# Performance work log

Measured on AMD Instinct MI355X. Metric: run time of the kernel, lower is better.

Reference implementation:

```python
import jax, jax.numpy as jnp
import numpy as np

HIDDEN = 768
NUM_HEADS = 12
HEAD_DIM = HIDDEN // NUM_HEADS


def setup_inputs() -> dict:
    key = jax.random.key(0)
    ks = jax.random.split(key, 10)
    B, S = 4, 2048
    scale = 1.0 / np.sqrt(HIDDEN)
    inp = {
        "hidden_states": jax.random.normal(ks[0], (B, S, HIDDEN), dtype=jnp.float32),
        "attention_mask": jnp.ones((B, S), dtype=jnp.float32),
        "Wq": jax.random.normal(ks[1], (HIDDEN, HIDDEN), dtype=jnp.float32) * scale,
        "bq": jnp.zeros((HIDDEN,), dtype=jnp.float32),
        "Wk": jax.random.normal(ks[2], (HIDDEN, HIDDEN), dtype=jnp.float32) * scale,
        "bk": jnp.zeros((HIDDEN,), dtype=jnp.float32),
        "Wv": jax.random.normal(ks[3], (HIDDEN, HIDDEN), dtype=jnp.float32) * scale,
        "bv": jnp.zeros((HIDDEN,), dtype=jnp.float32),
        "Wo": jax.random.normal(ks[4], (HIDDEN, HIDDEN), dtype=jnp.float32) * scale,
        "bo": jnp.zeros((HIDDEN,), dtype=jnp.float32),
    }
    return inp


def _split_heads(x):
    # [B,S,H] -> [B,nh,S,dh]
    B, S, _ = x.shape
    return x.reshape(B, S, NUM_HEADS, HEAD_DIM).transpose(0, 2, 1, 3)


def reference(hidden_states, attention_mask, Wq, bq, Wk, bk, Wv, bv, Wo, bo):
    # Linear projections (torch nn.Linear: x @ W.T + b; here W stored as [in,out])
    q = _split_heads(hidden_states @ Wq + bq)
    k = _split_heads(hidden_states @ Wk + bk)
    v = _split_heads(hidden_states @ Wv + bv)

    # scores: [B,nh,S,S]
    scores = jnp.einsum("bhqd,bhkd->bhqk", q, k) / np.sqrt(HEAD_DIM).astype(np.float32)

    # outer-product mask: [B,1,S,S], broadcast over heads
    ext = (attention_mask[:, :, None] * attention_mask[:, None, :])[:, None, :, :]
    scores = ext * scores - (1.0 - ext) * 1e9

    probs = jax.nn.softmax(scores, axis=-1)
    ctx = jnp.einsum("bhqk,bhkd->bhqd", probs, v)  # [B,nh,S,dh]
    B, _, S, _ = ctx.shape
    ctx = ctx.transpose(0, 2, 1, 3).reshape(B, S, HIDDEN)
    out = ctx @ Wo + bo
    # torch F.gelu default: exact (erf-based)
    return jax.nn.gelu(out, approximate=False)
```

## Files before the change

kernel.cpp:

```cpp
#include <hip/hip_runtime.h>
#include <math.h>

#define HIDDEN 768
#define NH 12
#define DH 64
#define SEQ 2048
#define BATCH 4

typedef __bf16 bf16;
typedef bf16 bf16x4 __attribute__((ext_vector_type(4)));
typedef bf16 bf16x8 __attribute__((ext_vector_type(8)));
typedef float f32x4 __attribute__((ext_vector_type(4)));

__device__ __forceinline__ void load_lds16(const void* g, void* l) {
    __builtin_amdgcn_global_load_lds(
        (__attribute__((address_space(1))) void*)g,
        (__attribute__((address_space(3))) void*)l, 16, 0, 0);
}

__global__ __launch_bounds__(256) void prep_xw(
    const float* __restrict__ X, bf16* __restrict__ Xb,
    const float* __restrict__ Wq, const float* __restrict__ Wk,
    const float* __restrict__ Wv, const float* __restrict__ Wo,
    bf16* __restrict__ Wt, bf16* __restrict__ Wot_hi,
    bf16* __restrict__ Wot_lo) {
    const int bid = blockIdx.x;
    const int tid = threadIdx.x;

    if (bid < 3072) {
        const size_t i = ((size_t)bid * 256 + tid) * 8;
        float4 a = *(const float4*)(X + i);
        float4 b = *(const float4*)(X + i + 4);
        bf16x8 o = {(bf16)a.x, (bf16)a.y, (bf16)a.z, (bf16)a.w,
                    (bf16)b.x, (bf16)b.y, (bf16)b.z, (bf16)b.w};
        *(bf16x8*)(Xb + i) = o;
        return;
    }

    __shared__ float Ts[64][68];
    const int r = bid - 3072;
    const int z = r / 144;
    const int rem = r - z * 144;
    const int n0 = (rem % 12) * 64, k0 = (rem / 12) * 64;
    const float* W = (z == 0) ? Wq : (z == 1) ? Wk : (z == 2) ? Wv : Wo;

    {
        const int rr = tid >> 2, c = (tid & 3) << 4;
        const float* src = W + (size_t)(k0 + rr) * HIDDEN + n0 + c;
#pragma unroll
        for (int j = 0; j < 4; ++j)
            *(float4*)&Ts[rr][c + 4 * j] = *(const float4*)(src + 4 * j);
    }
    __syncthreads();

    const int nl = tid >> 2, kc = (tid & 3) << 4;
    float v[16];
#pragma unroll
    for (int j = 0; j < 16; ++j) v[j] = Ts[kc + j][nl];

    if (z < 3) {
        bf16 hi[16];
#pragma unroll
        for (int j = 0; j < 16; ++j) hi[j] = (bf16)v[j];
        const size_t off = (size_t)(z * HIDDEN + n0 + nl) * HIDDEN + k0 + kc;
        *(bf16x8*)(Wt + off) = *(bf16x8*)&hi[0];
        *(bf16x8*)(Wt + off + 8) = *(bf16x8*)&hi[8];
    } else {
        bf16 hi[16], lo[16];
#pragma unroll
        for (int j = 0; j < 16; ++j) {
            hi[j] = (bf16)v[j];
            lo[j] = (bf16)(v[j] - (float)hi[j]);
        }
        const size_t off = (size_t)(n0 + nl) * HIDDEN + k0 + kc;
        *(bf16x8*)(Wot_hi + off) = *(bf16x8*)&hi[0];
        *(bf16x8*)(Wot_hi + off + 8) = *(bf16x8*)&hi[8];
        *(bf16x8*)(Wot_lo + off) = *(bf16x8*)&lo[0];
        *(bf16x8*)(Wot_lo + off + 8) = *(bf16x8*)&lo[8];
    }
}

__global__ __launch_bounds__(256, 3) void gemm_qkv(
    const bf16* __restrict__ Xb, const bf16* __restrict__ Wt,
    const float* __restrict__ bq, const float* __restrict__ bk,
    const float* __restrict__ bv, bf16* __restrict__ q_out,
    bf16* __restrict__ k_out, bf16* __restrict__ v_out) {
    __shared__ bf16 As[128 * 64];
    __shared__ bf16 Bs[192 * 64];

    const int tid = threadIdx.x;
    const int ln = tid & 63, wv = tid >> 6;
    const int quad = ln >> 4, l16 = ln & 15;
    const int wm = wv >> 1, wn = wv & 1;

    const int wg = blockIdx.x;
    const int xcd = wg & 7, i6 = wg >> 3;
    const int n0 = (i6 % 12) * 192;
    const int m0 = (xcd * 8 + i6 / 12) * 128;

    f32x4 acc[4][6];
#pragma unroll
    for (int i = 0; i < 4; ++i)
#pragma unroll
        for (int j = 0; j < 6; ++j) acc[i][j] = (f32x4){0.f, 0.f, 0.f, 0.f};

    const int r8 = ln >> 3;
    const int bcol_sw = ((ln & 7) << 4) ^ (r8 << 4);
    const char* gA =
        (const char*)Xb + ((size_t)(m0 + wv * 32 + r8) * HIDDEN) * 2 + bcol_sw;
    const char* gB =
        (const char*)Wt + ((size_t)(n0 + wv * 48 + r8) * HIDDEN) * 2 + bcol_sw;
    bf16* As_w = As + (wv * 32) * 64;
    bf16* Bs_w = Bs + (wv * 48) * 64;

    const int fsw = (l16 & 7) << 4;

    for (int k0 = 0; k0 < HIDDEN; k0 += 64) {
        __syncthreads();
#pragma unroll
        for (int j = 0; j < 4; ++j)
            load_lds16(gA + (size_t)k0 * 2 + (size_t)j * (8 * HIDDEN * 2),
                       As_w + j * 8 * 64);
#pragma unroll
        for (int j = 0; j < 6; ++j)
            load_lds16(gB + (size_t)k0 * 2 + (size_t)j * (8 * HIDDEN * 2),
                       Bs_w + j * 8 * 64);
        __syncthreads();

#pragma unroll
        for (int kk = 0; kk < 2; ++kk) {
            const int kb = kk * 64;
            bf16x8 ah[4], bh[6];
#pragma unroll
            for (int i = 0; i < 4; ++i)
                ah[i] = *(const bf16x8*)((const char*)As +
                                         (wm * 64 + i * 16 + l16) * 128 +
                                         ((kb + quad * 16) ^ fsw));
#pragma unroll
            for (int i = 0; i < 6; ++i)
                bh[i] = *(const bf16x8*)((const char*)Bs +
                                         (wn * 96 + i * 16 + l16) * 128 +
                                         ((kb + quad * 16) ^ fsw));
#pragma unroll
            for (int mi = 0; mi < 4; ++mi)
#pragma unroll
                for (int ni = 0; ni < 6; ++ni)
                    acc[mi][ni] = __builtin_amdgcn_mfma_f32_16x16x32_bf16(
                        ah[mi], bh[ni], acc[mi][ni], 0, 0, 0);
        }
    }

    const int nb = n0 + wn * 96;
    const int which = nb / HIDDEN;
    const int nrel = nb - which * HIDDEN;

    if (which < 2) {
        const float scale = (which == 0) ? 0.18033688011112042f : 1.0f;
        const float* bias = (which == 0) ? bq : bk;
        bf16* dst = (which == 0) ? q_out : k_out;
#pragma unroll
        for (int ni = 0; ni < 6; ++ni) {
            const int nn = nrel + ni * 16;
            const int h = nn >> 6;
            const int dh = (nn & 63) + l16;
            const float bb = bias[nn + l16];
#pragma unroll
            for (int mi = 0; mi < 4; ++mi)
#pragma unroll
                for (int r = 0; r < 4; ++r) {
                    const int m = m0 + wm * 64 + mi * 16 + quad * 4 + r;
                    const int bi = m >> 11, s = m & (SEQ - 1);
                    dst[(((size_t)(bi * NH + h) * SEQ + s) << 6) + dh] =
                        (bf16)(scale * (acc[mi][ni][r] + bb));
                }
        }
    } else {
        const int bi = m0 >> 11;
        const int sbase = (m0 & (SEQ - 1)) + wm * 64;
#pragma unroll
        for (int ni = 0; ni < 6; ++ni) {
            const int nn = nrel + ni * 16;
            const int h = nn >> 6;
            const int dh = (nn & 63) + l16;
            const float bb = bv[nn + l16];
            bf16* vrow = v_out + ((size_t)(bi * NH + h) * DH + dh) * SEQ;
#pragma unroll
            for (int mi = 0; mi < 4; ++mi) {
                bf16x4 pk = {(bf16)(acc[mi][ni][0] + bb),
                             (bf16)(acc[mi][ni][1] + bb),
                             (bf16)(acc[mi][ni][2] + bb),
                             (bf16)(acc[mi][ni][3] + bb)};
                *(bf16x4*)(vrow + sbase + mi * 16 + quad * 4) = pk;
            }
        }
    }
}

__global__ __launch_bounds__(256) void attn_mfma(const bf16* __restrict__ Q,
                                                 const bf16* __restrict__ K,
                                                 const bf16* __restrict__ Vt,
                                                 const float* __restrict__ mask,
                                                 bf16* __restrict__ ctx_hi,
                                                 bf16* __restrict__ ctx_lo) {
    __shared__ bf16 Ks[64 * 64];
    __shared__ bf16 Vts[64 * 64];
    __shared__ bf16 Ps[128 * 64];
    __shared__ float Ms[SEQ];
    __shared__ int allones_s;

    const int tid = threadIdx.x;
    const int ln = tid & 63, w = tid >> 6;
    const int quad = ln >> 4, l16 = ln & 15;

    const int wg = blockIdx.x;
    const int logical = (wg & 7) * 96 + (wg >> 3);
    const int qt = logical & 15;
    const int h = (logical >> 4) % NH;
    const int b = logical / (16 * NH);

    const size_t bh = (size_t)b * NH + h;
    const bf16* Qp = Q + ((bh * SEQ + (size_t)qt * 128) << 6);
    const bf16* Kp = K + (bh * SEQ << 6);
    const bf16* Vp = Vt + (bh * DH) * SEQ;

    if (tid == 0) allones_s = 1;
    {
        float4 m0 = *(const float4*)(mask + (size_t)b * SEQ + tid * 8);
        float4 m1 = *(const float4*)(mask + (size_t)b * SEQ + tid * 8 + 4);
        *(float4*)&Ms[tid * 8] = m0;
        *(float4*)&Ms[tid * 8 + 4] = m1;
        bool ok = (m0.x == 1.f) & (m0.y == 1.f) & (m0.z == 1.f) &
                  (m0.w == 1.f) & (m1.x == 1.f) & (m1.y == 1.f) &
                  (m1.z == 1.f) & (m1.w == 1.f);
        __syncthreads();
        if (!ok) allones_s = 0;
    }
    __syncthreads();
    const bool fastmask = (allones_s != 0);

    bf16x8 qb[2][2];
#pragma unroll
    for (int qg = 0; qg < 2; ++qg)
#pragma unroll
        for (int hf = 0; hf < 2; ++hf)
            qb[qg][hf] = *(const bf16x8*)(Qp + ((w * 32 + qg * 16 + l16) << 6) +
                                          hf * 32 + quad * 8);
    float mq[2];
#pragma unroll
    for (int qg = 0; qg < 2; ++qg)
        mq[qg] = Ms[qt * 128 + w * 32 + qg * 16 + l16];

    float l_i[2] = {0.f, 0.f};
    f32x4 acc[4][2];
#pragma unroll
    for (int fd = 0; fd < 4; ++fd)
#pragma unroll
        for (int qg = 0; qg < 2; ++qg) acc[fd][qg] = (f32x4){0.f, 0.f, 0.f, 0.f};

    const int sr = tid >> 2, sc = (tid & 3) << 4;
    const int ssw = (sr & 7) << 3;
    const int d0 = sc ^ ssw, d1 = (sc + 8) ^ ssw;
    const bf16* kbase = Kp + ((size_t)sr << 6) + sc;
    const bf16* vbase = Vp + (size_t)sr * SEQ + sc;

    bf16x8 kr0, kr1, vr0, vr1;
    kr0 = *(const bf16x8*)kbase;
    kr1 = *(const bf16x8*)(kbase + 8);
    vr0 = *(const bf16x8*)vbase;
    vr1 = *(const bf16x8*)(vbase + 8);

    for (int kt = 0; kt < SEQ / 64; ++kt) {
        __syncthreads();
        *(bf16x8*)&Ks[sr * 64 + d0] = kr0;
        *(bf16x8*)&Ks[sr * 64 + d1] = kr1;
        *(bf16x8*)&Vts[sr * 64 + d0] = vr0;
        *(bf16x8*)&Vts[sr * 64 + d1] = vr1;
        __syncthreads();
        if (kt + 1 < SEQ / 64) {
            kr0 = *(const bf16x8*)(kbase + ((size_t)(kt + 1) << 12));
            kr1 = *(const bf16x8*)(kbase + ((size_t)(kt + 1) << 12) + 8);
            vr0 = *(const bf16x8*)(vbase + (kt + 1) * 64);
            vr1 = *(const bf16x8*)(vbase + (kt + 1) * 64 + 8);
        }

        const int fsw = (l16 & 7) << 3;
        f32x4 st[4][2];
#pragma unroll
        for (int f = 0; f < 4; ++f) {
            const int krow = (f * 16 + l16) * 64;
            bf16x8 ka0 = *(bf16x8*)&Ks[krow + ((quad * 8) ^ fsw)];
            bf16x8 ka1 = *(bf16x8*)&Ks[krow + ((32 + quad * 8) ^ fsw)];
#pragma unroll
            for (int qg = 0; qg < 2; ++qg) {
                f32x4 c = {0.f, 0.f, 0.f, 0.f};
                c = __builtin_amdgcn_mfma_f32_16x16x32_bf16(ka0, qb[qg][0], c, 0, 0, 0);
                c = __builtin_amdgcn_mfma_f32_16x16x32_bf16(ka1, qb[qg][1], c, 0, 0, 0);
                st[f][qg] = c;
            }
        }

        if (!fastmask) {
#pragma unroll
            for (int f = 0; f < 4; ++f) {
                const float4 mk4 = *(const float4*)&Ms[kt * 64 + f * 16 + quad * 4];
                const float mkk[4] = {mk4.x, mk4.y, mk4.z, mk4.w};
#pragma unroll
                for (int qg = 0; qg < 2; ++qg)
#pragma unroll
                    for (int r = 0; r < 4; ++r) {
                        const float ext = mq[qg] * mkk[r];
                        st[f][qg][r] =
                            ext * st[f][qg][r] - (1.0f - ext) * 1.4426950e9f;
                    }
            }
        }

#pragma unroll
        for (int qg = 0; qg < 2; ++qg) {
            const int row = w * 32 + qg * 16 + l16;
            const int sw = (row & 7) << 3;
            bf16* prow = &Ps[row * 64];
#pragma unroll
            for (int f = 0; f < 4; ++f) {
                float p0 = __builtin_amdgcn_exp2f(st[f][qg][0]);
                float p1 = __builtin_amdgcn_exp2f(st[f][qg][1]);
                float p2 = __builtin_amdgcn_exp2f(st[f][qg][2]);
                float p3 = __builtin_amdgcn_exp2f(st[f][qg][3]);
                l_i[qg] += (p0 + p1) + (p2 + p3);
                bf16x4 pk = {(bf16)p0, (bf16)p1, (bf16)p2, (bf16)p3};
                *(bf16x4*)&prow[(f * 16 + quad * 4) ^ sw] = pk;
            }
        }

        bf16x8 pb[2][2];
#pragma unroll
        for (int qg = 0; qg < 2; ++qg) {
            const int row = w * 32 + qg * 16 + l16;
            const int sw = (row & 7) << 3;
#pragma unroll
            for (int hf = 0; hf < 2; ++hf)
                pb[qg][hf] =
                    *(bf16x8*)&Ps[row * 64 + ((hf * 32 + quad * 8) ^ sw)];
        }
#pragma unroll
        for (int fd = 0; fd < 4; ++fd) {
            const int vrow = (fd * 16 + l16) * 64;
            bf16x8 va0 = *(bf16x8*)&Vts[vrow + ((quad * 8) ^ fsw)];
            bf16x8 va1 = *(bf16x8*)&Vts[vrow + ((32 + quad * 8) ^ fsw)];
#pragma unroll
            for (int qg = 0; qg < 2; ++qg) {
                f32x4 c = acc[fd][qg];
                c = __builtin_amdgcn_mfma_f32_16x16x32_bf16(va0, pb[qg][0], c, 0, 0, 0);
                c = __builtin_amdgcn_mfma_f32_16x16x32_bf16(va1, pb[qg][1], c, 0, 0, 0);
                acc[fd][qg] = c;
            }
        }
    }

#pragma unroll
    for (int qg = 0; qg < 2; ++qg) {
        l_i[qg] += __shfl_xor(l_i[qg], 16);
        l_i[qg] += __shfl_xor(l_i[qg], 32);
    }

#pragma unroll
    for (int qg = 0; qg < 2; ++qg) {
        const float inv = 1.0f / l_i[qg];
        const size_t row = (size_t)b * SEQ + qt * 128 + w * 32 + qg * 16 + l16;
#pragma unroll
        for (int fd = 0; fd < 4; ++fd) {
            bf16 hi[4], lo[4];
#pragma unroll
            for (int r = 0; r < 4; ++r) {
                const float o = acc[fd][qg][r] * inv;
                hi[r] = (bf16)o;
                lo[r] = (bf16)(o - (float)hi[r]);
            }
            const size_t off = row * HIDDEN + h * 64 + fd * 16 + quad * 4;
            *(bf16x4*)(ctx_hi + off) = *(bf16x4*)&hi[0];
            *(bf16x4*)(ctx_lo + off) = *(bf16x4*)&lo[0];
        }
    }
}

__global__ __launch_bounds__(256) void gemm_out(const bf16* __restrict__ Ah,
                                                const bf16* __restrict__ Al,
                                                const bf16* __restrict__ Bhi,
                                                const bf16* __restrict__ Blo,
                                                const float* __restrict__ bo,
                                                float* __restrict__ fout) {
    __shared__ bf16 As_hi[128 * 64];
    __shared__ bf16 As_lo[128 * 64];
    __shared__ bf16 Bs_hi[64 * 64];
    __shared__ bf16 Bs_lo[64 * 64];

    const int tid = threadIdx.x;
    const int ln = tid & 63, wv = tid >> 6;
    const int quad = ln >> 4, l16 = ln & 15;
    const int wm = wv >> 1, wn = wv & 1;

    const int wg = blockIdx.x;
    const int xcd = wg & 7, i6 = wg >> 3;
    const int n0 = (i6 % 12) * 64;
    const int m0 = (xcd * 8 + i6 / 12) * 128;

    f32x4 acc[4][2];
#pragma unroll
    for (int i = 0; i < 4; ++i)
#pragma unroll
        for (int j = 0; j < 2; ++j) acc[i][j] = (f32x4){0.f, 0.f, 0.f, 0.f};

    const int r8 = ln >> 3;
    const int bcol_sw = ((ln & 7) << 4) ^ (r8 << 4);
    const char* gAh =
        (const char*)Ah + ((size_t)(m0 + wv * 32 + r8) * HIDDEN) * 2 + bcol_sw;
    const char* gAl =
        (const char*)Al + ((size_t)(m0 + wv * 32 + r8) * HIDDEN) * 2 + bcol_sw;
    const char* gBh =
        (const char*)Bhi + ((size_t)(n0 + wv * 16 + r8) * HIDDEN) * 2 + bcol_sw;
    const char* gBl =
        (const char*)Blo + ((size_t)(n0 + wv * 16 + r8) * HIDDEN) * 2 + bcol_sw;
    bf16* Ash_w = As_hi + (wv * 32) * 64;
    bf16* Asl_w = As_lo + (wv * 32) * 64;
    bf16* Bsh_w = Bs_hi + (wv * 16) * 64;
    bf16* Bsl_w = Bs_lo + (wv * 16) * 64;

    const int fsw = (l16 & 7) << 4;

    for (int k0 = 0; k0 < HIDDEN; k0 += 64) {
        __syncthreads();
#pragma unroll
        for (int j = 0; j < 4; ++j) {
            load_lds16(gAh + (size_t)k0 * 2 + (size_t)j * (8 * HIDDEN * 2),
                       Ash_w + j * 8 * 64);
            load_lds16(gAl + (size_t)k0 * 2 + (size_t)j * (8 * HIDDEN * 2),
                       Asl_w + j * 8 * 64);
        }
#pragma unroll
        for (int j = 0; j < 2; ++j) {
            load_lds16(gBh + (size_t)k0 * 2 + (size_t)j * (8 * HIDDEN * 2),
                       Bsh_w + j * 8 * 64);
            load_lds16(gBl + (size_t)k0 * 2 + (size_t)j * (8 * HIDDEN * 2),
                       Bsl_w + j * 8 * 64);
        }
        __syncthreads();

#pragma unroll
        for (int kk = 0; kk < 2; ++kk) {
            const int kb = kk * 64;
            bf16x8 ah[4], al[4], bh[2], bl[2];
#pragma unroll
            for (int i = 0; i < 4; ++i) {
                const int row = (wm * 64 + i * 16 + l16) * 128;
                ah[i] = *(const bf16x8*)((const char*)As_hi + row +
                                         ((kb + quad * 16) ^ fsw));
                al[i] = *(const bf16x8*)((const char*)As_lo + row +
                                         ((kb + quad * 16) ^ fsw));
            }
#pragma unroll
            for (int i = 0; i < 2; ++i) {
                const int row = (wn * 32 + i * 16 + l16) * 128;
                bh[i] = *(const bf16x8*)((const char*)Bs_hi + row +
                                         ((kb + quad * 16) ^ fsw));
                bl[i] = *(const bf16x8*)((const char*)Bs_lo + row +
                                         ((kb + quad * 16) ^ fsw));
            }
#pragma unroll
            for (int mi = 0; mi < 4; ++mi)
#pragma unroll
                for (int ni = 0; ni < 2; ++ni) {
                    f32x4 c = acc[mi][ni];
                    c = __builtin_amdgcn_mfma_f32_16x16x32_bf16(ah[mi], bh[ni],
                                                                c, 0, 0, 0);
                    c = __builtin_amdgcn_mfma_f32_16x16x32_bf16(ah[mi], bl[ni],
                                                                c, 0, 0, 0);
                    c = __builtin_amdgcn_mfma_f32_16x16x32_bf16(al[mi], bh[ni],
                                                                c, 0, 0, 0);
                    acc[mi][ni] = c;
                }
        }
    }

#pragma unroll
    for (int ni = 0; ni < 2; ++ni) {
        const int n = n0 + wn * 32 + ni * 16 + l16;
        const float bb = bo[n];
#pragma unroll
        for (int mi = 0; mi < 4; ++mi)
#pragma unroll
            for (int r = 0; r < 4; ++r) {
                const int m = m0 + wm * 64 + mi * 16 + quad * 4 + r;
                float x = acc[mi][ni][r] + bb;
                x = 0.5f * x * (1.0f + erff(x * 0.70710678118654752440f));
                fout[(size_t)m * HIDDEN + n] = x;
            }
    }
}

extern "C" void kernel_launch(void* const* d_in, const int* in_sizes, int n_in,
                              void* d_out, int out_size, void* d_ws, size_t ws_size,
                              hipStream_t stream) {
    const float* X    = (const float*)d_in[0];
    const float* mask = (const float*)d_in[1];
    const float* Wq   = (const float*)d_in[2];
    const float* bq   = (const float*)d_in[3];
    const float* Wk   = (const float*)d_in[4];
    const float* bk   = (const float*)d_in[5];
    const float* Wv   = (const float*)d_in[6];
    const float* bv   = (const float*)d_in[7];
    const float* Wo   = (const float*)d_in[8];
    const float* bo   = (const float*)d_in[9];
    float* out = (float*)d_out;

    char* w = (char*)d_ws;
    const size_t NE = (size_t)BATCH * SEQ * HIDDEN;
    bf16* q_ws   = (bf16*)w;  w += NE * 2;
    bf16* k_ws   = (bf16*)w;  w += NE * 2;
    bf16* vt_ws  = (bf16*)w;  w += NE * 2;
    bf16* ctx_hi = (bf16*)w;  w += NE * 2;
    bf16* ctx_lo = (bf16*)w;  w += NE * 2;
    bf16* Xb     = (bf16*)w;  w += NE * 2;
    bf16* Wt     = (bf16*)w;  w += (size_t)3 * HIDDEN * HIDDEN * 2;
    bf16* Wot_hi = (bf16*)w;  w += (size_t)HIDDEN * HIDDEN * 2;
    bf16* Wot_lo = (bf16*)w;  w += (size_t)HIDDEN * HIDDEN * 2;

    prep_xw<<<3648, 256, 0, stream>>>(X, Xb, Wq, Wk, Wv, Wo, Wt, Wot_hi,
                                      Wot_lo);
    gemm_qkv<<<dim3(768), 256, 0, stream>>>(Xb, Wt, bq, bk, bv, q_ws, k_ws,
                                            vt_ws);
    attn_mfma<<<dim3(16 * NH * BATCH), 256, 0, stream>>>(
        q_ws, k_ws, vt_ws, mask, ctx_hi, ctx_lo);
    gemm_out<<<dim3(768), 256, 0, stream>>>(ctx_hi, ctx_lo, Wot_hi, Wot_lo,
                                            bo, out);
}
```

Before: 251.3 us.

## Double-buffer LDS tiles with K=32 stages in QKV and output GEMMs

Both projection GEMMs switch from a single 64-wide K tile loaded and consumed between two barriers to two 32-wide K buffers in LDS. The next stage's global-to-LDS loads are issued before computing on the current buffer, so memory latency can overlap MFMA work. The XOR swizzle is redone for 64-byte rows. Each barrier now covers half as much compute, and the barrier count per K sweep stays the same (24), so sync overhead per FLOP goes up.

```diff
diff --git a/kernel.cpp b/kernel.cpp
--- a/kernel.cpp
+++ b/kernel.cpp
@@ -85,8 +85,8 @@
     const float* __restrict__ bq, const float* __restrict__ bk,
     const float* __restrict__ bv, bf16* __restrict__ q_out,
     bf16* __restrict__ k_out, bf16* __restrict__ v_out) {
-    __shared__ bf16 As[128 * 64];
-    __shared__ bf16 Bs[192 * 64];
+    __shared__ bf16 As[2][128 * 32];
+    __shared__ bf16 Bs[2][192 * 32];
 
     const int tid = threadIdx.x;
     const int ln = tid & 63, wv = tid >> 6;
@@ -104,50 +104,56 @@
 #pragma unroll
         for (int j = 0; j < 6; ++j) acc[i][j] = (f32x4){0.f, 0.f, 0.f, 0.f};
 
-    const int r8 = ln >> 3;
-    const int bcol_sw = ((ln & 7) << 4) ^ (r8 << 4);
+    const int srow = ln >> 2;
+    const int bcol_sw = ((ln & 3) << 4) ^ (((ln >> 3) & 3) << 4);
     const char* gA =
-        (const char*)Xb + ((size_t)(m0 + wv * 32 + r8) * HIDDEN) * 2 + bcol_sw;
+        (const char*)Xb + ((size_t)(m0 + wv * 32 + srow) * HIDDEN) * 2 + bcol_sw;
     const char* gB =
-        (const char*)Wt + ((size_t)(n0 + wv * 48 + r8) * HIDDEN) * 2 + bcol_sw;
-    bf16* As_w = As + (wv * 32) * 64;
-    bf16* Bs_w = Bs + (wv * 48) * 64;
-
-    const int fsw = (l16 & 7) << 4;
-
-    for (int k0 = 0; k0 < HIDDEN; k0 += 64) {
-        __syncthreads();
-#pragma unroll
-        for (int j = 0; j < 4; ++j)
-            load_lds16(gA + (size_t)k0 * 2 + (size_t)j * (8 * HIDDEN * 2),
-                       As_w + j * 8 * 64);
-#pragma unroll
-        for (int j = 0; j < 6; ++j)
-            load_lds16(gB + (size_t)k0 * 2 + (size_t)j * (8 * HIDDEN * 2),
-                       Bs_w + j * 8 * 64);
-        __syncthreads();
-
-#pragma unroll
-        for (int kk = 0; kk < 2; ++kk) {
-            const int kb = kk * 64;
-            bf16x8 ah[4], bh[6];
-#pragma unroll
-            for (int i = 0; i < 4; ++i)
-                ah[i] = *(const bf16x8*)((const char*)As +
-                                         (wm * 64 + i * 16 + l16) * 128 +
-                                         ((kb + quad * 16) ^ fsw));
-#pragma unroll
-            for (int i = 0; i < 6; ++i)
-                bh[i] = *(const bf16x8*)((const char*)Bs +
-                                         (wn * 96 + i * 16 + l16) * 128 +
-                                         ((kb + quad * 16) ^ fsw));
-#pragma unroll
-            for (int mi = 0; mi < 4; ++mi)
-#pragma unroll
-                for (int ni = 0; ni < 6; ++ni)
-                    acc[mi][ni] = __builtin_amdgcn_mfma_f32_16x16x32_bf16(
-                        ah[mi], bh[ni], acc[mi][ni], 0, 0, 0);
-        }
+        (const char*)Wt + ((size_t)(n0 + wv * 48 + srow) * HIDDEN) * 2 + bcol_sw;
+
+    const int fsw = ((l16 >> 1) & 3) << 4;
+
+    auto STAGE = [&](int b, int k0) {
+#pragma unroll
+        for (int j = 0; j < 2; ++j)
+            load_lds16(gA + (size_t)k0 * 2 + (size_t)j * (16 * HIDDEN * 2),
+                       &As[b][(wv * 32 + j * 16) * 32]);
+#pragma unroll
+        for (int j = 0; j < 3; ++j)
+            load_lds16(gB + (size_t)k0 * 2 + (size_t)j * (16 * HIDDEN * 2),
+                       &Bs[b][(wv * 48 + j * 16) * 32]);
+    };
+
+    auto COMPUTE = [&](int b) {
+        bf16x8 ah[4], bh[6];
+#pragma unroll
+        for (int i = 0; i < 4; ++i)
+            ah[i] = *(const bf16x8*)((const char*)&As[b][0] +
+                                     (wm * 64 + i * 16 + l16) * 64 +
+                                     ((quad * 16) ^ fsw));
+#pragma unroll
+        for (int i = 0; i < 6; ++i)
+            bh[i] = *(const bf16x8*)((const char*)&Bs[b][0] +
+                                     (wn * 96 + i * 16 + l16) * 64 +
+                                     ((quad * 16) ^ fsw));
+#pragma unroll
+        for (int mi = 0; mi < 4; ++mi)
+#pragma unroll
+            for (int ni = 0; ni < 6; ++ni)
+                acc[mi][ni] = __builtin_amdgcn_mfma_f32_16x16x32_bf16(
+                    ah[mi], bh[ni], acc[mi][ni], 0, 0, 0);
+    };
+
+    STAGE(0, 0);
+    __syncthreads();
+
+    for (int step = 0; step < 24; step += 2) {
+        if (step + 1 < 24) STAGE(1, (step + 1) * 32);
+        COMPUTE(0);
+        __syncthreads();
+        if (step + 2 < 24) STAGE(0, (step + 2) * 32);
+        COMPUTE(1);
+        __syncthreads();
     }
 
     const int nb = n0 + wn * 96;
@@ -389,10 +395,10 @@
                                                 const bf16* __restrict__ Blo,
                                                 const float* __restrict__ bo,
                                                 float* __restrict__ fout) {
-    __shared__ bf16 As_hi[128 * 64];
-    __shared__ bf16 As_lo[128 * 64];
-    __shared__ bf16 Bs_hi[64 * 64];
-    __shared__ bf16 Bs_lo[64 * 64];
+    __shared__ bf16 Ash[2][128 * 32];
+    __shared__ bf16 Asl[2][128 * 32];
+    __shared__ bf16 Bsh[2][64 * 32];
+    __shared__ bf16 Bsl[2][64 * 32];
 
     const int tid = threadIdx.x;
     const int ln = tid & 63, wv = tid >> 6;
@@ -410,75 +416,71 @@
 #pragma unroll
         for (int j = 0; j < 2; ++j) acc[i][j] = (f32x4){0.f, 0.f, 0.f, 0.f};
 
-    const int r8 = ln >> 3;
-    const int bcol_sw = ((ln & 7) << 4) ^ (r8 << 4);
+    const int srow = ln >> 2;
+    const int bcol_sw = ((ln & 3) << 4) ^ (((ln >> 3) & 3) << 4);
     const char* gAh =
-        (const char*)Ah + ((size_t)(m0 + wv * 32 + r8) * HIDDEN) * 2 + bcol_sw;
+        (const char*)Ah + ((size_t)(m0 + wv * 32 + srow) * HIDDEN) * 2 + bcol_sw;
     const char* gAl =
-        (const char*)Al + ((size_t)(m0 + wv * 32 + r8) * HIDDEN) * 2 + bcol_sw;
+        (const char*)Al + ((size_t)(m0 + wv * 32 + srow) * HIDDEN) * 2 + bcol_sw;
     const char* gBh =
-        (const char*)Bhi + ((size_t)(n0 + wv * 16 + r8) * HIDDEN) * 2 + bcol_sw;
+        (const char*)Bhi + ((size_t)(n0 + wv * 16 + srow) * HIDDEN) * 2 + bcol_sw;
     const char* gBl =
-        (const char*)Blo + ((size_t)(n0 + wv * 16 + r8) * HIDDEN) * 2 + bcol_sw;
-    bf16* Ash_w = As_hi + (wv * 32) * 64;
-    bf16* Asl_w = As_lo + (wv * 32) * 64;
-    bf16* Bsh_w = Bs_hi + (wv * 16) * 64;
-    bf16* Bsl_w = Bs_lo + (wv * 16) * 64;
-
-    const int fsw = (l16 & 7) << 4;
-
-    for (int k0 = 0; k0 < HIDDEN; k0 += 64) {
-        __syncthreads();
-#pragma unroll
-        for (int j = 0; j < 4; ++j) {
-            load_lds16(gAh + (size_t)k0 * 2 + (size_t)j * (8 * HIDDEN * 2),
-                       Ash_w + j * 8 * 64);
-            load_lds16(gAl + (size_t)k0 * 2 + (size_t)j * (8 * HIDDEN * 2),
-                       Asl_w + j * 8 * 64);
-        }
+        (const char*)Blo + ((size_t)(n0 + wv * 16 + srow) * HIDDEN) * 2 + bcol_sw;
+
+    const int fsw = ((l16 >> 1) & 3) << 4;
+
+    auto STAGE = [&](int b, int k0) {
 #pragma unroll
         for (int j = 0; j < 2; ++j) {
-            load_lds16(gBh + (size_t)k0 * 2 + (size_t)j * (8 * HIDDEN * 2),
-                       Bsh_w + j * 8 * 64);
-            load_lds16(gBl + (size_t)k0 * 2 + (size_t)j * (8 * HIDDEN * 2),
-                       Bsl_w + j * 8 * 64);
-        }
-        __syncthreads();
-
-#pragma unroll
-        for (int kk = 0; kk < 2; ++kk) {
-            const int kb = kk * 64;
-            bf16x8 ah[4], al[4], bh[2], bl[2];
-#pragma unroll
-            for (int i = 0; i < 4; ++i) {
-                const int row = (wm * 64 + i * 16 + l16) * 128;
-                ah[i] = *(const bf16x8*)((const char*)As_hi + row +
-                                         ((kb + quad * 16) ^ fsw));
-                al[i] = *(const bf16x8*)((const char*)As_lo + row +
-                                         ((kb + quad * 16) ^ fsw));
-            }
-#pragma unroll
-            for (int i = 0; i < 2; ++i) {
-                const int row = (wn * 32 + i * 16 + l16) * 128;
-                bh[i] = *(const bf16x8*)((const char*)Bs_hi + row +
-                                         ((kb + quad * 16) ^ fsw));
-                bl[i] = *(const bf16x8*)((const char*)Bs_lo + row +
-                                         ((kb + quad * 16) ^ fsw));
-            }
-#pragma unroll
-            for (int mi = 0; mi < 4; ++mi)
-#pragma unroll
-                for (int ni = 0; ni < 2; ++ni) {
-                    f32x4 c = acc[mi][ni];
-                    c = __builtin_amdgcn_mfma_f32_16x16x32_bf16(ah[mi], bh[ni],
-                                                                c, 0, 0, 0);
-                    c = __builtin_amdgcn_mfma_f32_16x16x32_bf16(ah[mi], bl[ni],
-                                                                c, 0, 0, 0);
-                    c = __builtin_amdgcn_mfma_f32_16x16x32_bf16(al[mi], bh[ni],
-                                                                c, 0, 0, 0);
-                    acc[mi][ni] = c;
-                }
-        }
+            load_lds16(gAh + (size_t)k0 * 2 + (size_t)j * (16 * HIDDEN * 2),
+                       &Ash[b][(wv * 32 + j * 16) * 32]);
+            load_lds16(gAl + (size_t)k0 * 2 + (size_t)j * (16 * HIDDEN * 2),
+                       &Asl[b][(wv * 32 + j * 16) * 32]);
+        }
+        load_lds16(gBh + (size_t)k0 * 2, &Bsh[b][(wv * 16) * 32]);
+        load_lds16(gBl + (size_t)k0 * 2, &Bsl[b][(wv * 16) * 32]);
+    };
+
+    auto COMPUTE = [&](int b) {
+        bf16x8 ah[4], al[4], bh[2], bl[2];
+#pragma unroll
+        for (int i = 0; i < 4; ++i) {
+            const int row = (wm * 64 + i * 16 + l16) * 64;
+            ah[i] = *(const bf16x8*)((const char*)&Ash[b][0] + row +
+                                     ((quad * 16) ^ fsw));
+            al[i] = *(const bf16x8*)((const char*)&Asl[b][0] + row +
+                                     ((quad * 16) ^ fsw));
+        }
+#pragma unroll
+        for (int i = 0; i < 2; ++i) {
+            const int row = (wn * 32 + i * 16 + l16) * 64;
+            bh[i] = *(const bf16x8*)((const char*)&Bsh[b][0] + row +
+                                     ((quad * 16) ^ fsw));
+            bl[i] = *(const bf16x8*)((const char*)&Bsl[b][0] + row +
+                                     ((quad * 16) ^ fsw));
+        }
+#pragma unroll
+        for (int mi = 0; mi < 4; ++mi)
+#pragma unroll
+            for (int ni = 0; ni < 2; ++ni) {
+                f32x4 c = acc[mi][ni];
+                c = __builtin_amdgcn_mfma_f32_16x16x32_bf16(ah[mi], bh[ni], c, 0, 0, 0);
+                c = __builtin_amdgcn_mfma_f32_16x16x32_bf16(ah[mi], bl[ni], c, 0, 0, 0);
+                c = __builtin_amdgcn_mfma_f32_16x16x32_bf16(al[mi], bh[ni], c, 0, 0, 0);
+                acc[mi][ni] = c;
+            }
+    };
+
+    STAGE(0, 0);
+    __syncthreads();
+
+    for (int step = 0; step < 24; step += 2) {
+        if (step + 1 < 24) STAGE(1, (step + 1) * 32);
+        COMPUTE(0);
+        __syncthreads();
+        if (step + 2 < 24) STAGE(0, (step + 2) * 32);
+        COMPUTE(1);
+        __syncthreads();
     }
 
 #pragma unroll
```

Result: no change. 248.4 us (median of 3 runs) (-1.2%).
